# Kernel optimization log

Hardware: AMD Instinct MI355X
Metric: run time of the kernel (lower is better)

## Reference

```python
import jax, jax.numpy as jnp
import numpy as np

EPS_DIST = 1e-10
BN_EPS = 1e-5
K = 3  # nsample / three_nn


def setup_inputs() -> dict:
    key = jax.random.key(0)
    ks = jax.random.split(key, 8)
    B, N, S, D1, D2 = 4, 8192, 2048, 128, 256
    C_in = D1 + D2  # 384
    H = 256
    inp = {
        "pos1": jax.random.normal(ks[0], (B, 3, N), dtype=jnp.float32),
        "pos2": jax.random.normal(ks[1], (B, 3, S), dtype=jnp.float32),
        "feature1": jax.random.normal(ks[2], (B, D1, N), dtype=jnp.float32),
        "feature2": jax.random.normal(ks[3], (B, D2, S), dtype=jnp.float32),
        # MLP layer 1: Conv1d(384->256, k=1) + BN
        "W1": jax.random.normal(ks[4], (H, C_in), dtype=jnp.float32) * (1.0 / np.sqrt(C_in)),
        "b1": jnp.zeros((H,), dtype=jnp.float32),
        "g1": jnp.ones((H,), dtype=jnp.float32),
        "be1": jnp.zeros((H,), dtype=jnp.float32),
        # MLP layer 2: Conv1d(256->256, k=1) + BN
        "W2": jax.random.normal(ks[5], (H, H), dtype=jnp.float32) * (1.0 / np.sqrt(H)),
        "b2": jnp.zeros((H,), dtype=jnp.float32),
        "g2": jnp.ones((H,), dtype=jnp.float32),
        "be2": jnp.zeros((H,), dtype=jnp.float32),
    }
    return inp


def _conv_bn_relu(x, W, b, gamma, beta):
    # x: [B, Cin, N]; 1x1 Conv1d == channel GEMM
    y = jnp.einsum("oc,bcn->bon", W, x) + b[None, :, None]
    # BatchNorm1d in training mode: batch statistics over (B, N)
    mean = jnp.mean(y, axis=(0, 2), keepdims=True)
    var = jnp.mean(jnp.square(y - mean), axis=(0, 2), keepdims=True)
    y = (y - mean) * jax.lax.rsqrt(var + BN_EPS)
    y = y * gamma[None, :, None] + beta[None, :, None]
    return jax.nn.relu(y)


def reference(pos1, pos2, feature1, feature2, W1, b1, g1, be1, W2, b2, g2, be2):
    # pos1: [B,3,N], pos2: [B,3,S], feature1: [B,D1,N], feature2: [B,D2,S]
    p1 = jnp.swapaxes(pos1, 1, 2)  # [B,N,3]
    p2 = jnp.swapaxes(pos2, 1, 2)  # [B,S,3]
    # three_nn: squared-distance 3-NN of each point in p1 among p2
    d2 = (jnp.sum(p1 * p1, -1)[:, :, None]
          + jnp.sum(p2 * p2, -1)[:, None, :]
          - 2.0 * jnp.einsum("bnc,bsc->bns", p1, p2))  # [B,N,S]
    neg_vals, idx = jax.lax.top_k(-d2, K)  # idx: [B,N,3]
    dists = jnp.maximum(-neg_vals, EPS_DIST)  # dists[dists<1e-10]=1e-10
    w = 1.0 / dists
    w = w / jnp.sum(w, -1, keepdims=True)  # [B,N,3]
    # grouping_operation: gather feature2 [B,D,S] by idx -> [B,D,N,3]
    grouped = jax.vmap(lambda f, i: f[:, i])(feature2, idx)
    interpolated = jnp.sum(grouped * w[:, None, :, :], axis=-1)  # [B,D2,N]
    feat = jnp.concatenate([interpolated, feature1], axis=1)  # [B,384,N]
    feat = _conv_bn_relu(feat, W1, b1, g1, be1)
    feat = _conv_bn_relu(feat, W2, b2, g2, be2)
    return feat  # [B,256,N]
```

## Files before the change

### kernel.cpp

```cpp
#include <hip/hip_runtime.h>
#include <hip/hip_bf16.h>
#include <cstdint>

typedef unsigned short u16;
typedef unsigned int u32;
typedef unsigned long long u64;
typedef __bf16 bf16x8 __attribute__((ext_vector_type(8)));
typedef float f32x4 __attribute__((ext_vector_type(4)));
typedef u16 u16x8 __attribute__((ext_vector_type(8)));

__device__ __forceinline__ u16 f2b(float f) {
    unsigned int u = __float_as_uint(f);
    u += 0x7fffu + ((u >> 16) & 1u);
    return (u16)(u >> 16);
}
__device__ __forceinline__ float b2f(u16 h) {
    return __uint_as_float(((unsigned int)h) << 16);
}
__device__ __forceinline__ void async_cp16(void* lds, const void* g) {
    __builtin_amdgcn_global_load_lds((const __attribute__((address_space(1))) void*)g,
                                     (__attribute__((address_space(3))) void*)lds, 16, 0, 0);
}
__device__ __forceinline__ u32 fmono(float f) {
    u32 u = __float_as_uint(f);
    return u ^ (((u32)((int)u >> 31)) | 0x80000000u);
}
__device__ __forceinline__ u64 shfl_xor_u64(u64 v, int mask) {
    u32 lo = (u32)v, hi = (u32)(v >> 32);
    lo = (u32)__shfl_xor((int)lo, mask);
    hi = (u32)__shfl_xor((int)hi, mask);
    return ((u64)hi << 32) | lo;
}
__device__ __forceinline__ void ins3(u64 k, u64& k0, u64& k1, u64& k2) {
    bool c0 = k > k0, c1 = k > k1, c2 = k > k2;
    k2 = c1 ? k1 : (c2 ? k : k2);
    k1 = c0 ? k0 : (c1 ? k : k1);
    k0 = c0 ? k : k0;
}
__device__ __forceinline__ int pkix(int i) { return i + (i >> 6); }

#define NB_NN  512
#define NB_CVT 160
#define NB_T2  512
#define NB_T1  1024

__global__ __launch_bounds__(256, 4) void prep_kernel(const float* __restrict__ w1,
                                                      const float* __restrict__ w2,
                                                      u16* __restrict__ wb,
                                                      const float* __restrict__ feature2,
                                                      u16* __restrict__ f2t,
                                                      const float* __restrict__ feature1,
                                                      u16* __restrict__ f1t,
                                                      const float* __restrict__ pos1,
                                                      const float* __restrict__ pos2,
                                                      int* __restrict__ idx_out,
                                                      float* __restrict__ w_out) {
    __shared__ __align__(16) char smem[22784];
    int bi = blockIdx.x;
    int tid = threadIdx.x;

    if (bi >= NB_NN) {
        int ci = bi - NB_NN;
        if (ci < NB_CVT) {
            int i = ci * 256 + tid;
            if (i < 40960) {
                const float* src = (i < 24576) ? w1 : w2;
                int k = (i < 24576) ? i : (i - 24576);
                float4 v = *(const float4*)&src[(size_t)k * 4];
                ushort4 o;
                o.x = f2b(v.x); o.y = f2b(v.y); o.z = f2b(v.z); o.w = f2b(v.w);
                *(ushort4*)&wb[(size_t)i * 4] = o;
            }
            return;
        }
        float (*t)[65] = (float (*)[65])smem;
        const float* in; u16* out; int C, S, s0, c0, b;
        if (ci < NB_CVT + NB_T2) {
            int lin = ci - NB_CVT;
            C = 256; S = 2048; in = feature2; out = f2t;
            s0 = (lin & 31) * 64; c0 = ((lin >> 5) & 3) * 64; b = lin >> 7;
        } else {
            int lin = ci - NB_CVT - NB_T2;
            C = 128; S = 8192; in = feature1; out = f1t;
            s0 = (lin & 127) * 64; c0 = ((lin >> 7) & 1) * 64; b = lin >> 8;
        }
        const float* ib = in + (size_t)b * C * S;
        u16* ob = out + (size_t)b * S * C;
        int col = tid & 63, r0 = tid >> 6;
#pragma unroll
        for (int p = 0; p < 16; ++p) {
            int c = p * 4 + r0;
            t[c][col] = ib[(size_t)(c0 + c) * S + s0 + col];
        }
        __syncthreads();
#pragma unroll
        for (int p = 0; p < 16; ++p) {
            int s = p * 4 + r0;
            ob[(size_t)(s0 + s) * C + c0 + col] = f2b(t[col][s]);
        }
        return;
    }

    float4* pk = (float4*)smem;
    u64* warr = (u64*)(smem + 16640);
    int j0 = bi * 64;
    int b = j0 >> 13;
    const float* p2 = pos2 + (size_t)b * 3 * 2048;
    int p = tid & 15, ck = tid >> 4;
    int wv = tid >> 6, lane = tid & 63;
    const float* p1 = pos1 + (size_t)b * 3 * 8192;
    float qx[4], qy[4], qz[4];
#pragma unroll
    for (int t = 0; t < 4; ++t) {
        int n = (j0 & 8191) + p + t * 16;
        qx[t] = p1[n]; qy[t] = p1[8192 + n]; qz[t] = p1[16384 + n];
    }
    u64 key[4][3];
#pragma unroll
    for (int t = 0; t < 4; ++t) { key[t][0] = 0; key[t][1] = 0; key[t][2] = 0; }

    for (int half = 0; half < 2; ++half) {
        int hbase = half * 1024;
        for (int i = tid; i < 1024; i += 256) {
            int s = hbase + i;
            float x = p2[s], y = p2[2048 + s], z = p2[4096 + s];
            pk[pkix(i)] = make_float4(x, y, z, -0.5f * (x * x + y * y + z * z));
        }
        __syncthreads();

        float g[4][3]; int id[4][3];
#pragma unroll
        for (int t = 0; t < 4; ++t) {
            g[t][0] = -3.4e38f; g[t][1] = -3.4e38f; g[t][2] = -3.4e38f;
            id[t][0] = 0; id[t][1] = 0; id[t][2] = 0;
        }
        int sb = ck * 64;
        const float4* pc = pk + pkix(sb);
#pragma unroll 2
        for (int it = 0; it < 64; ++it) {
            float4 cd = pc[it];
            int s = sb + it;
#pragma unroll
            for (int t = 0; t < 4; ++t) {
                float tv = fmaf(qx[t], cd.x, fmaf(qy[t], cd.y, fmaf(qz[t], cd.z, cd.w)));
                bool c0 = tv > g[t][0], c1 = tv > g[t][1], c2 = tv > g[t][2];
                g[t][2] = c1 ? g[t][1] : (c2 ? tv : g[t][2]);
                id[t][2] = c1 ? id[t][1] : (c2 ? s : id[t][2]);
                g[t][1] = c0 ? g[t][0] : (c1 ? tv : g[t][1]);
                id[t][1] = c0 ? id[t][0] : (c1 ? s : id[t][1]);
                g[t][0] = c0 ? tv : g[t][0];
                id[t][0] = c0 ? s : id[t][0];
            }
        }
        __syncthreads();

#pragma unroll
        for (int t = 0; t < 4; ++t) {
#pragma unroll
            for (int r = 0; r < 3; ++r)
                ins3(((u64)fmono(g[t][r]) << 32) | (u64)(2047 - (hbase + id[t][r])),
                     key[t][0], key[t][1], key[t][2]);
        }
    }

#pragma unroll
    for (int mask = 16; mask <= 32; mask <<= 1) {
#pragma unroll
        for (int t = 0; t < 4; ++t) {
            u64 m0 = shfl_xor_u64(key[t][0], mask);
            u64 m1 = shfl_xor_u64(key[t][1], mask);
            u64 m2 = shfl_xor_u64(key[t][2], mask);
            ins3(m0, key[t][0], key[t][1], key[t][2]);
            ins3(m1, key[t][0], key[t][1], key[t][2]);
            ins3(m2, key[t][0], key[t][1], key[t][2]);
        }
    }
    if (lane < 16) {
        u64* wr = &warr[(wv * 16 + p) * 12];
#pragma unroll
        for (int t = 0; t < 4; ++t) {
            wr[t * 3 + 0] = key[t][0]; wr[t * 3 + 1] = key[t][1]; wr[t * 3 + 2] = key[t][2];
        }
    }
    __syncthreads();
    if (tid < 64) {
        int pp = tid & 15, t = tid >> 4;
        const u64* w0 = &warr[pp * 12 + t * 3];
        u64 k0 = w0[0], k1 = w0[1], k2 = w0[2];
#pragma unroll
        for (int w = 1; w < 4; ++w) {
            const u64* wr = &warr[(w * 16 + pp) * 12 + t * 3];
            ins3(wr[0], k0, k1, k2);
            ins3(wr[1], k0, k1, k2);
            ins3(wr[2], k0, k1, k2);
        }
        int s0 = 2047 - (int)(k0 & 0xFFFFFFFFu);
        int s1 = 2047 - (int)(k1 & 0xFFFFFFFFu);
        int s2 = 2047 - (int)(k2 & 0xFFFFFFFFu);
        int j = j0 + pp + t * 16;
        int n = j & 8191;
        float x1 = p1[n], y1 = p1[8192 + n], z1 = p1[16384 + n];
        float n1 = x1 * x1 + y1 * y1 + z1 * z1;
        float X0 = p2[s0], Y0 = p2[2048 + s0], Z0 = p2[4096 + s0];
        float X1 = p2[s1], Y1v = p2[2048 + s1], Z1 = p2[4096 + s1];
        float X2 = p2[s2], Y2v = p2[2048 + s2], Z2 = p2[4096 + s2];
        float t0 = x1 * X0 + y1 * Y0 + z1 * Z0 - 0.5f * (X0 * X0 + Y0 * Y0 + Z0 * Z0);
        float t1 = x1 * X1 + y1 * Y1v + z1 * Z1 - 0.5f * (X1 * X1 + Y1v * Y1v + Z1 * Z1);
        float t2 = x1 * X2 + y1 * Y2v + z1 * Z2 - 0.5f * (X2 * X2 + Y2v * Y2v + Z2 * Z2);
        float d0 = fmaxf(fmaf(-2.f, t0, n1), 1e-10f);
        float d1 = fmaxf(fmaf(-2.f, t1, n1), 1e-10f);
        float d2 = fmaxf(fmaf(-2.f, t2, n1), 1e-10f);
        float w0v = 1.f / d0, w1v = 1.f / d1, w2v = 1.f / d2;
        float inv = 1.f / (w0v + w1v + w2v);
        idx_out[j * 3] = s0; idx_out[j * 3 + 1] = s1; idx_out[j * 3 + 2] = s2;
        w_out[j * 3] = w0v * inv; w_out[j * 3 + 1] = w1v * inv; w_out[j * 3 + 2] = w2v * inv;
    }
}

template <int KT, bool GATHER, bool FUSE>
__global__ __launch_bounds__(256, 2) void gemm_kernel(const u16* __restrict__ A1,
                                                      const u16* __restrict__ A2,
                                                      const u16* __restrict__ Bw,
                                                      const float* __restrict__ bias,
                                                      const int* __restrict__ idx,
                                                      const float* __restrict__ wgt,
                                                      const float* __restrict__ stats_in,
                                                      const float* __restrict__ g_in,
                                                      const float* __restrict__ be_in,
                                                      u16* __restrict__ Yb,
                                                      float* __restrict__ stats) {
    __shared__ __align__(16) char smemA[36864];
    u16* Al = (u16*)smemA;
    u16* Bl = (u16*)(smemA + 16384);
    u16* T  = (u16*)smemA;
    float2* BNT = (float2*)(smemA + 34816);
    int tid = threadIdx.x;
    int lane = tid & 63, wv = tid >> 6;
    int j0 = blockIdx.x * 128, m0 = blockIdx.y * 128;
    int l15 = lane & 15, q = lane >> 4;
    int wj = (wv >> 1) * 64, wm = (wv & 1) * 64;
    f32x4 acc[4][4];
#pragma unroll
    for (int i = 0; i < 4; ++i)
#pragma unroll
        for (int jj = 0; jj < 4; ++jj) acc[i][jj] = (f32x4){0.f, 0.f, 0.f, 0.f};

    int rbase = wv * 32;
    int lrow = lane >> 3, lchunk = lane & 7;
    int schunk = lchunk ^ lrow;
    const u16* Bg = Bw + (size_t)m0 * KT;

    if (FUSE) {
        int m = tid;
        const float inv = 1.f / 32768.f;
        float mean = stats_in[m] * inv;
        float var = stats_in[256 + m] * inv - mean * mean;
        float a = g_in[m] * rsqrtf(var + 1e-5f);
        BNT[m] = make_float2(a, be_in[m] - mean * a);
        __syncthreads();
    }

    const u16* grow0[4]; const u16* grow1[4]; const u16* grow2[4];
    float gw0[4], gw1[4], gw2[4];
    if (GATHER) {
#pragma unroll
        for (int qq = 0; qq < 4; ++qq) {
            int jl = rbase + qq * 8 + lrow;
            int j = j0 + jl;
            int bb = j >> 13;
            const u16* fb = A1 + (size_t)bb * 2048 * 256;
            grow0[qq] = fb + (size_t)idx[j * 3 + 0] * 256;
            grow1[qq] = fb + (size_t)idx[j * 3 + 1] * 256;
            grow2[qq] = fb + (size_t)idx[j * 3 + 2] * 256;
            gw0[qq] = wgt[j * 3 + 0]; gw1[qq] = wgt[j * 3 + 1]; gw2[qq] = wgt[j * 3 + 2];
        }
    }

    for (int k0 = 0; k0 < KT; k0 += 64) {
#pragma unroll
        for (int qq = 0; qq < 4; ++qq) {
            int row = rbase + qq * 8;
            async_cp16(&Bl[row * 64], Bg + (size_t)(row + lrow) * KT + k0 + schunk * 8);
        }
        if (GATHER && k0 < 256) {
            int c = k0 + lchunk * 8;
#pragma unroll
            for (int qq = 0; qq < 4; ++qq) {
                int row = rbase + qq * 8;
                u16x8 v0 = *(const u16x8*)(grow0[qq] + c);
                u16x8 v1 = *(const u16x8*)(grow1[qq] + c);
                u16x8 v2 = *(const u16x8*)(grow2[qq] + c);
                u16x8 o;
#pragma unroll
                for (int e = 0; e < 8; ++e)
                    o[e] = f2b(gw0[qq] * b2f(v0[e]) + gw1[qq] * b2f(v1[e]) + gw2[qq] * b2f(v2[e]));
                *(u16x8*)&Al[(row + lrow) * 64 + schunk * 8] = o;
            }
        } else if (FUSE) {
            int c = k0 + lchunk * 8;
            float2 bn[8];
#pragma unroll
            for (int e = 0; e < 8; ++e) bn[e] = BNT[c + e];
#pragma unroll
            for (int qq = 0; qq < 4; ++qq) {
                int row = rbase + qq * 8;
                u16x8 y = *(const u16x8*)&A1[(size_t)(j0 + row + lrow) * 256 + c];
                u16x8 o;
#pragma unroll
                for (int e = 0; e < 8; ++e)
                    o[e] = f2b(fmaxf(b2f(y[e]) * bn[e].x + bn[e].y, 0.f));
                *(u16x8*)&Al[(row + lrow) * 64 + schunk * 8] = o;
            }
        } else {
            const u16* src = A2 + (size_t)j0 * 128 + (k0 - 256);
#pragma unroll
            for (int qq = 0; qq < 4; ++qq) {
                int row = rbase + qq * 8;
                async_cp16(&Al[row * 64], src + (size_t)(row + lrow) * 128 + schunk * 8);
            }
        }
        __syncthreads();
#pragma unroll
        for (int ks = 0; ks < 2; ++ks) {
            bf16x8 af[4], bfr[4];
#pragma unroll
            for (int i = 0; i < 4; ++i) {
                int row = wj + i * 16 + l15;
                af[i] = *(const bf16x8*)&Al[row * 64 + ((ks * 4 + q) ^ (l15 & 7)) * 8];
            }
#pragma unroll
            for (int i = 0; i < 4; ++i) {
                int row = wm + i * 16 + l15;
                bfr[i] = *(const bf16x8*)&Bl[row * 64 + ((ks * 4 + q) ^ (l15 & 7)) * 8];
            }
#pragma unroll
            for (int i = 0; i < 4; ++i)
#pragma unroll
                for (int jj = 0; jj < 4; ++jj)
                    acc[i][jj] = __builtin_amdgcn_mfma_f32_16x16x32_bf16(af[i], bfr[jj],
                                                                         acc[i][jj], 0, 0, 0);
        }
        __syncthreads();
    }
#pragma unroll
    for (int jj = 0; jj < 4; ++jj) {
        int ml = wm + jj * 16 + l15;
        float bv = bias[m0 + ml];
        float s = 0.f, s2 = 0.f;
#pragma unroll
        for (int i = 0; i < 4; ++i) {
            int jl = wj + i * 16 + q * 4;
#pragma unroll
            for (int r = 0; r < 4; ++r) {
                float v = acc[i][jj][r] + bv;
                s += v; s2 += v * v;
                T[(jl + r) * 136 + ml] = f2b(v);
            }
        }
        s += __shfl_xor(s, 16); s += __shfl_xor(s, 32);
        s2 += __shfl_xor(s2, 16); s2 += __shfl_xor(s2, 32);
        if (q == 0) {
            atomicAdd(&stats[m0 + ml], s);
            atomicAdd(&stats[256 + m0 + ml], s2);
        }
    }
    __syncthreads();
#pragma unroll
    for (int it = 0; it < 8; ++it) {
        int jl = it * 16 + wv * 4 + q;
        u16x8 v = *(const u16x8*)&T[jl * 136 + l15 * 8];
        *(u16x8*)&Yb[(size_t)(j0 + jl) * 256 + m0 + l15 * 8] = v;
    }
}

__global__ __launch_bounds__(256) void final_out_kernel(const u16* __restrict__ Y2,
                                                        const float* __restrict__ stats,
                                                        const float* __restrict__ g,
                                                        const float* __restrict__ be,
                                                        float* __restrict__ out) {
    __shared__ float t[64][65];
    int j0 = blockIdx.x * 64, o0 = blockIdx.y * 64;
    int tid = threadIdx.x;
    int c4 = (tid & 15) * 4, rw = tid >> 4;
#pragma unroll
    for (int p = 0; p < 4; ++p) {
        int jl = p * 16 + rw;
        ushort4 v = *(const ushort4*)&Y2[(size_t)(j0 + jl) * 256 + o0 + c4];
        t[jl][c4] = b2f(v.x); t[jl][c4 + 1] = b2f(v.y);
        t[jl][c4 + 2] = b2f(v.z); t[jl][c4 + 3] = b2f(v.w);
    }
    __syncthreads();
    int b = j0 >> 13, n0 = j0 & 8191;
    const float inv = 1.f / 32768.f;
#pragma unroll
    for (int p = 0; p < 4; ++p) {
        int ol = p * 16 + rw;
        int o = o0 + ol;
        float mean = stats[o] * inv;
        float var = stats[256 + o] * inv - mean * mean;
        float a = g[o] * rsqrtf(var + 1e-5f);
        float s = be[o] - mean * a;
        float4 v;
        v.x = fmaxf(t[c4][ol] * a + s, 0.f);
        v.y = fmaxf(t[c4 + 1][ol] * a + s, 0.f);
        v.z = fmaxf(t[c4 + 2][ol] * a + s, 0.f);
        v.w = fmaxf(t[c4 + 3][ol] * a + s, 0.f);
        *(float4*)&out[(size_t)b * 2097152 + (size_t)o * 8192 + n0 + c4] = v;
    }
}

extern "C" void kernel_launch(void* const* d_in, const int* in_sizes, int n_in,
                              void* d_out, int out_size, void* d_ws, size_t ws_size,
                              hipStream_t stream) {
    const float* pos1 = (const float*)d_in[0];
    const float* pos2 = (const float*)d_in[1];
    const float* feature1 = (const float*)d_in[2];
    const float* feature2 = (const float*)d_in[3];
    const float* W1 = (const float*)d_in[4];
    const float* b1 = (const float*)d_in[5];
    const float* g1 = (const float*)d_in[6];
    const float* be1 = (const float*)d_in[7];
    const float* W2 = (const float*)d_in[8];
    const float* b2 = (const float*)d_in[9];
    const float* g2 = (const float*)d_in[10];
    const float* be2 = (const float*)d_in[11];

    char* ws = (char*)d_ws;
    int*   IDX    = (int*)(ws + 0);
    float* WGT    = (float*)(ws + 393216);
    u16*   W1B    = (u16*)(ws + 786432);
    u16*   W2B    = (u16*)(ws + 983040);
    float* STATS  = (float*)(ws + 1114112);
    u16*   F2T    = (u16*)(ws + 1118208);
    u16*   F1T    = (u16*)(ws + 5312512);
    u16*   Y1     = (u16*)(ws + 13701120);
    u16*   Y2     = (u16*)(ws + 30478336);
    float* OUT    = (float*)d_out;

    hipMemsetAsync(STATS, 0, 1024 * sizeof(float), stream);
    prep_kernel<<<NB_NN + NB_CVT + NB_T2 + NB_T1, 256, 0, stream>>>(
        W1, W2, W1B, feature2, F2T, feature1, F1T, pos1, pos2, IDX, WGT);
    gemm_kernel<384, true, false><<<dim3(256, 2), 256, 0, stream>>>(
        F2T, F1T, W1B, b1, IDX, WGT, nullptr, nullptr, nullptr, Y1, STATS);
    gemm_kernel<256, false, true><<<dim3(256, 2), 256, 0, stream>>>(
        Y1, nullptr, W2B, b2, nullptr, nullptr, STATS, g1, be1, Y2, STATS + 512);
    final_out_kernel<<<dim3(512, 4), 256, 0, stream>>>(Y2, STATS + 512, g2, be2, OUT);
}
```

Measured before the change: 199.5 us.

## Replace atomic BN stat accumulation with per-block partials and reduce kernel

GEMM blocks now write per-wave-pair partial sums and sums of squares to a partials buffer instead of doing float atomicAdds to a shared stats array. A small reduce kernel sums the partials and precomputes the BN scale and shift, which the next GEMM and the final kernel read directly. This removes atomic contention and the memset, and makes the statistics deterministic. In exchange it adds two extra kernel launches, and the reduce kernel runs on only 4 blocks with serial loops.

After: 188.6 us. 1.06x faster.

```diff
diff --git a/kernel.cpp b/kernel.cpp
--- a/kernel.cpp
+++ b/kernel.cpp
@@ -224,11 +224,9 @@
                                                       const float* __restrict__ bias,
                                                       const int* __restrict__ idx,
                                                       const float* __restrict__ wgt,
-                                                      const float* __restrict__ stats_in,
-                                                      const float* __restrict__ g_in,
-                                                      const float* __restrict__ be_in,
+                                                      const float2* __restrict__ bnt_in,
                                                       u16* __restrict__ Yb,
-                                                      float* __restrict__ stats) {
+                                                      float* __restrict__ Pt) {
     __shared__ __align__(16) char smemA[36864];
     u16* Al = (u16*)smemA;
     u16* Bl = (u16*)(smemA + 16384);
@@ -251,12 +249,7 @@
     const u16* Bg = Bw + (size_t)m0 * KT;
 
     if (FUSE) {
-        int m = tid;
-        const float inv = 1.f / 32768.f;
-        float mean = stats_in[m] * inv;
-        float var = stats_in[256 + m] * inv - mean * mean;
-        float a = g_in[m] * rsqrtf(var + 1e-5f);
-        BNT[m] = make_float2(a, be_in[m] - mean * a);
+        BNT[tid] = bnt_in[tid];
         __syncthreads();
     }
 
@@ -360,8 +353,9 @@
         s += __shfl_xor(s, 16); s += __shfl_xor(s, 32);
         s2 += __shfl_xor(s2, 16); s2 += __shfl_xor(s2, 32);
         if (q == 0) {
-            atomicAdd(&stats[m0 + ml], s);
-            atomicAdd(&stats[256 + m0 + ml], s2);
+            size_t prow = (size_t)blockIdx.x * 2 + (wv >> 1);
+            Pt[prow * 512 + (m0 + ml)] = s;
+            Pt[prow * 512 + 256 + (m0 + ml)] = s2;
         }
     }
     __syncthreads();
@@ -373,10 +367,35 @@
     }
 }
 
+__global__ __launch_bounds__(256) void reduce_kernel(const float* __restrict__ P,
+                                                     const float* __restrict__ g,
+                                                     const float* __restrict__ be,
+                                                     float2* __restrict__ bnt) {
+    __shared__ float ls[4][64], ls2[4][64];
+    int tid = threadIdx.x;
+    int ch = blockIdx.x * 64 + (tid & 63);
+    int rg = tid >> 6;
+    float s = 0.f, s2 = 0.f;
+    for (int r = rg * 128; r < rg * 128 + 128; ++r) {
+        s += P[(size_t)r * 512 + ch];
+        s2 += P[(size_t)r * 512 + 256 + ch];
+    }
+    ls[rg][tid & 63] = s; ls2[rg][tid & 63] = s2;
+    __syncthreads();
+    if (tid < 64) {
+        float fs = ls[0][tid] + ls[1][tid] + ls[2][tid] + ls[3][tid];
+        float fs2 = ls2[0][tid] + ls2[1][tid] + ls2[2][tid] + ls2[3][tid];
+        int c = blockIdx.x * 64 + tid;
+        const float inv = 1.f / 32768.f;
+        float mean = fs * inv;
+        float var = fs2 * inv - mean * mean;
+        float a = g[c] * rsqrtf(var + 1e-5f);
+        bnt[c] = make_float2(a, be[c] - mean * a);
+    }
+}
+
 __global__ __launch_bounds__(256) void final_out_kernel(const u16* __restrict__ Y2,
-                                                        const float* __restrict__ stats,
-                                                        const float* __restrict__ g,
-                                                        const float* __restrict__ be,
+                                                        const float2* __restrict__ bnt,
                                                         float* __restrict__ out) {
     __shared__ float t[64][65];
     int j0 = blockIdx.x * 64, o0 = blockIdx.y * 64;
@@ -391,15 +410,12 @@
     }
     __syncthreads();
     int b = j0 >> 13, n0 = j0 & 8191;
-    const float inv = 1.f / 32768.f;
 #pragma unroll
     for (int p = 0; p < 4; ++p) {
         int ol = p * 16 + rw;
         int o = o0 + ol;
-        float mean = stats[o] * inv;
-        float var = stats[256 + o] * inv - mean * mean;
-        float a = g[o] * rsqrtf(var + 1e-5f);
-        float s = be[o] - mean * a;
+        float2 bn = bnt[o];
+        float a = bn.x, s = bn.y;
         float4 v;
         v.x = fmaxf(t[c4][ol] * a + s, 0.f);
         v.y = fmaxf(t[c4 + 1][ol] * a + s, 0.f);
@@ -426,23 +442,27 @@
     const float* be2 = (const float*)d_in[11];
 
     char* ws = (char*)d_ws;
-    int*   IDX    = (int*)(ws + 0);
-    float* WGT    = (float*)(ws + 393216);
-    u16*   W1B    = (u16*)(ws + 786432);
-    u16*   W2B    = (u16*)(ws + 983040);
-    float* STATS  = (float*)(ws + 1114112);
-    u16*   F2T    = (u16*)(ws + 1118208);
-    u16*   F1T    = (u16*)(ws + 5312512);
-    u16*   Y1     = (u16*)(ws + 13701120);
-    u16*   Y2     = (u16*)(ws + 30478336);
-    float* OUT    = (float*)d_out;
-
-    hipMemsetAsync(STATS, 0, 1024 * sizeof(float), stream);
+    int*    IDX   = (int*)(ws + 0);
+    float*  WGT   = (float*)(ws + 393216);
+    u16*    W1B   = (u16*)(ws + 786432);
+    u16*    W2B   = (u16*)(ws + 983040);
+    float2* BNT1G = (float2*)(ws + 1114112);
+    float2* BNT2G = (float2*)(ws + 1116160);
+    u16*    F2T   = (u16*)(ws + 1118208);
+    u16*    F1T   = (u16*)(ws + 5312512);
+    u16*    Y1    = (u16*)(ws + 13701120);
+    u16*    Y2    = (u16*)(ws + 30478336);
+    float*  P1    = (float*)(ws + 47255552);
+    float*  P2    = (float*)(ws + 48304128);
+    float*  OUT   = (float*)d_out;
+
     prep_kernel<<<NB_NN + NB_CVT + NB_T2 + NB_T1, 256, 0, stream>>>(
         W1, W2, W1B, feature2, F2T, feature1, F1T, pos1, pos2, IDX, WGT);
     gemm_kernel<384, true, false><<<dim3(256, 2), 256, 0, stream>>>(
-        F2T, F1T, W1B, b1, IDX, WGT, nullptr, nullptr, nullptr, Y1, STATS);
+        F2T, F1T, W1B, b1, IDX, WGT, nullptr, Y1, P1);
+    reduce_kernel<<<4, 256, 0, stream>>>(P1, g1, be1, BNT1G);
     gemm_kernel<256, false, true><<<dim3(256, 2), 256, 0, stream>>>(
-        Y1, nullptr, W2B, b2, nullptr, nullptr, STATS, g1, be1, Y2, STATS + 512);
-    final_out_kernel<<<dim3(512, 4), 256, 0, stream>>>(Y2, STATS + 512, g2, be2, OUT);
-}
+        Y1, nullptr, W2B, b2, nullptr, nullptr, BNT1G, Y2, P2);
+    reduce_kernel<<<4, 256, 0, stream>>>(P2, g2, be2, BNT2G);
+    final_out_kernel<<<dim3(512, 4), 256, 0, stream>>>(Y2, BNT2G, OUT);
+}
```
